# Kernel optimization log

Measured on AMD Instinct MI355X. Metric: run time of the kernel, lower is better.

## Reference

```python
import jax, jax.numpy as jnp
import numpy as np
from jax import lax

S, B, D, H, NQ = 512, 2048, 128, 8, 8  # seq, batch, input_dim, hidden_dim(=n_qubits), n_qubits
EPS = 1e-5


def _qexp(theta):
    """Closed-form PauliZ expectations of the RY-ladder + CNOT-ring circuit.
    <Z_0> = prod_{j=1..n-1} cos(theta_j); <Z_i> = prod_{j=0..i} cos(theta_j) for i>=1.
    theta: [..., NQ] -> [..., NQ]."""
    c = jnp.cos(theta)
    cp = jnp.cumprod(c, axis=-1)                                  # cp[...,i] = prod_{0..i}
    out0 = jnp.prod(c[..., 1:], axis=-1, keepdims=True)           # prod_{1..n-1}
    return jnp.concatenate([out0, cp[..., 1:]], axis=-1)


def _layernorm(x, g, b):
    mu = jnp.mean(x, axis=-1, keepdims=True)
    var = jnp.mean(jnp.square(x - mu), axis=-1, keepdims=True)
    return (x - mu) * lax.rsqrt(var + EPS) * g + b


def setup_inputs() -> dict:
    key = jax.random.key(0)
    ks = jax.random.split(key, 10)
    inputs = jax.random.normal(ks[0], (S, B, D), jnp.float32)
    conv_w = jax.random.normal(ks[1], (H, D, 3), jnp.float32) * (1.0 / np.sqrt(3 * D))
    ln_g = jnp.ones((2 * H,), jnp.float32)
    ln_b = jnp.zeros((2 * H,), jnp.float32)

    def lin(k):
        k1, k2 = jax.random.split(k)
        W = jax.random.normal(k1, (NQ, 2 * H), jnp.float32) * (1.0 / np.sqrt(2 * H))
        b = jax.random.normal(k2, (NQ,), jnp.float32) * 0.05
        return W, b

    Wf, bf = lin(ks[2]); Wi, bi = lin(ks[3]); Wg, bg = lin(ks[4]); Wo, bo = lin(ks[5])
    return dict(inputs=inputs, conv_w=conv_w, ln_g=ln_g, ln_b=ln_b,
                Wf=Wf, bf=bf, Wi=Wi, bi=bi, Wg=Wg, bg=bg, Wo=Wo, bo=bo)


def reference(inputs, conv_w, ln_g, ln_b, Wf, bf, Wi, bi, Wg, bg, Wo, bo):
    # encoder: Conv1d(k=3, pad=1, no bias) over the sequence axis
    x = jnp.transpose(inputs, (1, 2, 0))                           # [B, D, S]
    enc = lax.conv_general_dilated(x, conv_w, window_strides=(1,), padding='SAME',
                                   dimension_numbers=('NCW', 'OIW', 'NCW'))  # [B, H, S]
    enc = jnp.transpose(enc, (2, 0, 1))                            # [S, B, H]

    hx0 = jnp.zeros((B, H), inputs.dtype)
    cx0 = jnp.zeros((B, H), inputs.dtype)

    def step(carry, x_t):
        hx, cx = carry
        comb = _layernorm(jnp.concatenate([x_t, hx], axis=1), ln_g, ln_b)  # [B, 2H]
        f = jax.nn.sigmoid(_qexp(comb @ Wf.T + bf))
        i = jax.nn.sigmoid(_qexp(comb @ Wi.T + bi))
        g = jnp.tanh(_qexp(comb @ Wg.T + bg))
        o = jax.nn.sigmoid(_qexp(comb @ Wo.T + bo))
        # dropout is identity in eval mode
        cx = f * cx + i * g
        hx = o * jnp.tanh(cx)
        return (hx, cx), hx

    (hx, cx), outputs = lax.scan(step, (hx0, cx0), enc)
    return outputs, hx, cx
```

## Files before the change

### kernel.cpp

```cpp
#include <hip/hip_runtime.h>

#define SS 512
#define BB 2048
#define DD 128
#define HH 8

template<int CTRL>
__device__ __forceinline__ float dppf(float old_, float src) {
  return __int_as_float(__builtin_amdgcn_update_dpp(
      __float_as_int(old_), __float_as_int(src), CTRL, 0xF, 0xF, false));
}

__global__ void kw_transpose(const float* __restrict__ w, float* __restrict__ wt) {
  int i = blockIdx.x * blockDim.x + threadIdx.x;
  if (i < 3 * DD * HH) {
    int k = i >> 10;
    int d = (i >> 3) & 127;
    int h = i & 7;
    wt[i] = w[h * (DD * 3) + d * 3 + k];
  }
}

__global__ __launch_bounds__(256) void kconv(const float* __restrict__ x,
                                             const float* __restrict__ wt,
                                             float* __restrict__ enc) {
  const int b = blockIdx.x * 256 + threadIdx.x;
  const int s = blockIdx.y;
  float acc0=0.f,acc1=0.f,acc2=0.f,acc3=0.f,acc4=0.f,acc5=0.f,acc6=0.f,acc7=0.f;

  auto proc = [&](float xe, const float* w8) {
    float4 wa = *(const float4*)(w8);
    float4 wb = *(const float4*)(w8 + 4);
    acc0 = fmaf(xe, wa.x, acc0); acc1 = fmaf(xe, wa.y, acc1);
    acc2 = fmaf(xe, wa.z, acc2); acc3 = fmaf(xe, wa.w, acc3);
    acc4 = fmaf(xe, wb.x, acc4); acc5 = fmaf(xe, wb.y, acc5);
    acc6 = fmaf(xe, wb.z, acc6); acc7 = fmaf(xe, wb.w, acc7);
  };

  #pragma unroll
  for (int k = 0; k < 3; ++k) {
    int sr = s + k - 1;
    if (sr >= 0 && sr < SS) {
      const float* xr = x + ((size_t)sr * BB + b) * DD;
      const float* wk = wt + k * (DD * HH);
      #pragma unroll 4
      for (int d = 0; d < DD; d += 4) {
        float4 xv = *(const float4*)(xr + d);
        const float* wp = wk + d * 8;
        proc(xv.x, wp);
        proc(xv.y, wp + 8);
        proc(xv.z, wp + 16);
        proc(xv.w, wp + 24);
      }
    }
  }
  float4* op = (float4*)(enc + ((size_t)s * BB + b) * HH);
  op[0] = make_float4(acc0, acc1, acc2, acc3);
  op[1] = make_float4(acc4, acc5, acc6, acc7);
}

__global__ __launch_bounds__(64) void krec(
    const float* __restrict__ ln_g, const float* __restrict__ ln_b,
    const float* __restrict__ Wf, const float* __restrict__ bf,
    const float* __restrict__ Wi, const float* __restrict__ bi,
    const float* __restrict__ Wg, const float* __restrict__ bg,
    const float* __restrict__ Wo, const float* __restrict__ bo,
    float* __restrict__ out)
{
  const int tid  = threadIdx.x;
  const int sub  = tid & 31;
  const int gate = sub >> 3;
  const int q    = sub & 7;
  const int b    = blockIdx.x * 2 + (tid >> 5);

  const float* Wm = (gate == 0) ? Wf : (gate == 1) ? Wi : (gate == 2) ? Wg : Wo;
  const float* bm = (gate == 0) ? bf : (gate == 1) ? bi : (gate == 2) ? bg : bo;

  float wraw[16];
  #pragma unroll
  for (int j = 0; j < 16; ++j) wraw[j] = Wm[q * 16 + j];
  float SWp = 0.f, bb = bm[q];
  #pragma unroll
  for (int j = 0; j < 16; ++j) {
    SWp += wraw[j] * ln_g[j];
    bb  = fmaf(ln_b[j], wraw[j], bb);
  }
  float wx[8], wh[8];
  #pragma unroll
  for (int j = 0; j < 8; ++j) wx[j] = wraw[j] * ln_g[j];
  #pragma unroll
  for (int k = 0; k < 8; ++k) { int src = 8 + (q ^ k); wh[k] = wraw[src] * ln_g[src]; }

  const bool  isG  = (gate == 2);
  const float ymul = isG ? 2.f : 1.f;
  const bool  gb0  = (gate & 1) != 0;
  const bool  gb1  = (gate & 2) != 0;

  float h_own = 0.f, c_own = 0.f;
  float r0=0.f,r1=0.f,r2=0.f,r3=0.f,r4=0.f,r5=0.f,r6=0.f,r7=0.f;

  const float4* pl = (const float4*)out + (size_t)b * 2;
  float4 cv0 = pl[0], cv1 = pl[1];
  float* pst = out + (size_t)b * 8 + q;

  for (int s = 0; s < SS; ++s) {
    const float x0=cv0.x, x1=cv0.y, x2=cv0.z, x3=cv0.w;
    const float x4=cv1.x, x5=cv1.y, x6=cv1.z, x7=cv1.w;
    if (s + 1 < SS) {
      pl += BB * 2;
      cv0 = pl[0]; cv1 = pl[1];
    }
    float sv = (((x0+x1)+(x2+x3)) + ((x4+x5)+(x6+x7)))
             + (((r0+r1)+(r2+r3)) + ((r4+r5)+(r6+r7)));
    float qa = fmaf(x0,x0, x1*x1) + fmaf(x2,x2, x3*x3);
    float qb = fmaf(x4,x4, x5*x5) + fmaf(x6,x6, x7*x7);
    float qc = fmaf(r0,r0, r1*r1) + fmaf(r2,r2, r3*r3);
    float qd = fmaf(r4,r4, r5*r5) + fmaf(r6,r6, r7*r7);
    float sq  = (qa + qb) + (qc + qd);
    float mu  = sv * 0.0625f;
    float var = fmaf(-mu, mu, sq * 0.0625f);
    float rinv = __builtin_amdgcn_rsqf(var + 1e-5f);
    float d0 = fmaf(x0,wx[0], x1*wx[1]); d0 = fmaf(x2,wx[2], d0); d0 = fmaf(x3,wx[3], d0);
    float d1 = fmaf(x4,wx[4], x5*wx[5]); d1 = fmaf(x6,wx[6], d1); d1 = fmaf(x7,wx[7], d1);
    float d2 = fmaf(r0,wh[0], r1*wh[1]); d2 = fmaf(r2,wh[2], d2); d2 = fmaf(r3,wh[3], d2);
    float d3 = fmaf(r4,wh[4], r5*wh[5]); d3 = fmaf(r6,wh[6], d3); d3 = fmaf(r7,wh[7], d3);
    float dot = (d0 + d1) + (d2 + d3);
    float theta = fmaf(fmaf(-mu, SWp, dot), rinv, bb);
    float c = __cosf(theta);
    float cp = (q == 0) ? 1.f : c;
    float t;
    t = dppf<0x111>(cp, cp); cp = (q >= 1) ? cp * t : cp;
    t = dppf<0x112>(cp, cp); cp = (q >= 2) ? cp * t : cp;
    t = dppf<0x114>(cp, cp); cp = (q >= 4) ? cp * t : cp;
    float cb  = dppf<0x00>(c, c);
    float cb2 = dppf<0x114>(cb, cb);
    float c0b = (q >= 4) ? cb2 : cb;
    float tot = dppf<0x141>(cp, cp);
    float outq = (q == 0) ? tot : c0b * cp;
    float e  = __expf(-(outq * ymul));
    float sg = __builtin_amdgcn_rcpf(1.f + e);
    float a  = isG ? fmaf(2.f, sg, -1.f) : sg;
    float t1 = dppf<0x128>(a, a);
    float t2 = __shfl_xor(a, 16);
    float t3 = __shfl_xor(t1, 16);
    float v01  = gb0 ? t1 : a;
    float v23  = gb0 ? t3 : t2;
    float v01i = gb0 ? a  : t1;
    float v23i = gb0 ? t2 : t3;
    float fv = gb1 ? v23  : v01;
    float gv = gb1 ? v01  : v23;
    float iv = gb1 ? v23i : v01i;
    float ov = gb1 ? v01i : v23i;
    c_own = fmaf(fv, c_own, iv * gv);
    float e2 = __expf(-2.f * c_own);
    float th = fmaf(2.f, __builtin_amdgcn_rcpf(1.f + e2), -1.f);
    h_own = ov * th;
    if (gate == 0) *pst = h_own;
    pst += BB * HH;
    r0 = h_own;
    r1 = dppf<0xB1>(r0, r0);
    r2 = dppf<0x4E>(r0, r0);
    r3 = dppf<0x4E>(r1, r1);
    float m0 = dppf<0x141>(r0, r0);
    float m1 = dppf<0x141>(r1, r1);
    float m2 = dppf<0x141>(r2, r2);
    float m3 = dppf<0x141>(r3, r3);
    r4 = dppf<0x1B>(m0, m0);
    r5 = dppf<0x1B>(m1, m1);
    r6 = dppf<0x1B>(m2, m2);
    r7 = dppf<0x1B>(m3, m3);
  }
  if (gate == 0) {
    out[(size_t)SS * BB * HH + (size_t)b * HH + q] = h_own;
    out[(size_t)SS * BB * HH + (size_t)BB * HH + (size_t)b * HH + q] = c_own;
  }
}

extern "C" void kernel_launch(void* const* d_in, const int* in_sizes, int n_in,
                              void* d_out, int out_size, void* d_ws, size_t ws_size,
                              hipStream_t stream) {
  const float* x   = (const float*)d_in[0];
  const float* cw  = (const float*)d_in[1];
  const float* lng = (const float*)d_in[2];
  const float* lnb = (const float*)d_in[3];
  const float* Wf_ = (const float*)d_in[4];
  const float* bf_ = (const float*)d_in[5];
  const float* Wi_ = (const float*)d_in[6];
  const float* bi_ = (const float*)d_in[7];
  const float* Wg_ = (const float*)d_in[8];
  const float* bg_ = (const float*)d_in[9];
  const float* Wo_ = (const float*)d_in[10];
  const float* bo_ = (const float*)d_in[11];
  float* out = (float*)d_out;
  float* wt  = (float*)d_ws;

  kw_transpose<<<12, 256, 0, stream>>>(cw, wt);
  kconv<<<dim3(BB / 256, SS), 256, 0, stream>>>(x, wt, out);
  krec<<<BB / 2, 64, 0, stream>>>(lng, lnb, Wf_, bf_, Wi_, bi_, Wg_, bg_, Wo_, bo_, out);
}
```

Measured before the change: 1.115 ms.

## Restructure conv to load each input row once with rolling accumulators and prefetch deeper in recurrence

The conv kernel now tiles 64 sequence rows per block. Each input row is read once and feeds three rolling accumulators for the three kernel taps, instead of being re-read three times. The weight transpose kernel is removed and weights go into LDS. Lanes split D into 4 chunks, with a DPP/swizzle reduction before the store. The recurrence kernel re-maps lanes so the gate exchange uses permlane32 swap instead of a shuffle, prefetches three timesteps ahead, and slightly rebalances the dot-product trees for ILP.

```diff
diff --git a/kernel.cpp b/kernel.cpp
--- a/kernel.cpp
+++ b/kernel.cpp
@@ -4,6 +4,7 @@
 #define BB 2048
 #define DD 128
 #define HH 8
+#define TS 64
 
 template<int CTRL>
 __device__ __forceinline__ float dppf(float old_, float src) {
@@ -11,52 +12,94 @@
       __float_as_int(old_), __float_as_int(src), CTRL, 0xF, 0xF, false));
 }
 
-__global__ void kw_transpose(const float* __restrict__ w, float* __restrict__ wt) {
-  int i = blockIdx.x * blockDim.x + threadIdx.x;
-  if (i < 3 * DD * HH) {
-    int k = i >> 10;
-    int d = (i >> 3) & 127;
-    int h = i & 7;
-    wt[i] = w[h * (DD * 3) + d * 3 + k];
-  }
+__device__ __forceinline__ float xorswap32(float v, bool hi) {
+#if __has_builtin(__builtin_amdgcn_permlane32_swap)
+  auto r = __builtin_amdgcn_permlane32_swap(__float_as_int(v), __float_as_int(v), false, false);
+  struct { int a, b; } s2;
+  __builtin_memcpy(&s2, &r, 8);
+  return __int_as_float(hi ? s2.a : s2.b);
+#else
+  return __shfl_xor(v, 32);
+#endif
 }
 
 __global__ __launch_bounds__(256) void kconv(const float* __restrict__ x,
-                                             const float* __restrict__ wt,
+                                             const float* __restrict__ cw,
                                              float* __restrict__ enc) {
-  const int b = blockIdx.x * 256 + threadIdx.x;
-  const int s = blockIdx.y;
-  float acc0=0.f,acc1=0.f,acc2=0.f,acc3=0.f,acc4=0.f,acc5=0.f,acc6=0.f,acc7=0.f;
-
-  auto proc = [&](float xe, const float* w8) {
-    float4 wa = *(const float4*)(w8);
-    float4 wb = *(const float4*)(w8 + 4);
-    acc0 = fmaf(xe, wa.x, acc0); acc1 = fmaf(xe, wa.y, acc1);
-    acc2 = fmaf(xe, wa.z, acc2); acc3 = fmaf(xe, wa.w, acc3);
-    acc4 = fmaf(xe, wb.x, acc4); acc5 = fmaf(xe, wb.y, acc5);
-    acc6 = fmaf(xe, wb.z, acc6); acc7 = fmaf(xe, wb.w, acc7);
-  };
-
-  #pragma unroll
-  for (int k = 0; k < 3; ++k) {
-    int sr = s + k - 1;
-    if (sr >= 0 && sr < SS) {
-      const float* xr = x + ((size_t)sr * BB + b) * DD;
-      const float* wk = wt + k * (DD * HH);
-      #pragma unroll 4
-      for (int d = 0; d < DD; d += 4) {
-        float4 xv = *(const float4*)(xr + d);
-        const float* wp = wk + d * 8;
-        proc(xv.x, wp);
-        proc(xv.y, wp + 8);
-        proc(xv.z, wp + 16);
-        proc(xv.w, wp + 24);
-      }
+  __shared__ float wl[3][8][132];
+  const int tid = threadIdx.x;
+  for (int i = tid; i < 3 * DD * HH; i += 256) {
+    int h = i / 384;
+    int rem = i - h * 384;
+    int d = rem / 3;
+    int k = rem - d * 3;
+    wl[k][h][d] = cw[i];
+  }
+  __syncthreads();
+
+  const int lane = tid & 63;
+  const int hl   = lane & 31;
+  const int h    = hl & 7;
+  const int dc   = hl >> 3;
+  const int wv   = tid >> 6;
+  const int b    = blockIdx.x * 8 + wv * 2 + (lane >> 5);
+  const int c0   = blockIdx.y * TS;
+  const int dbase = dc * 32;
+
+  auto loadrow = [&](int r, float4 (&xb)[8]) {
+    if (r >= 0 && r < SS) {
+      const float4* p = (const float4*)(x + ((size_t)r * BB + b) * DD + dbase);
+      #pragma unroll
+      for (int j = 0; j < 8; ++j) xb[j] = p[j];
+    } else {
+      #pragma unroll
+      for (int j = 0; j < 8; ++j) xb[j] = make_float4(0.f, 0.f, 0.f, 0.f);
     }
-  }
-  float4* op = (float4*)(enc + ((size_t)s * BB + b) * HH);
-  op[0] = make_float4(acc0, acc1, acc2, acc3);
-  op[1] = make_float4(acc4, acc5, acc6, acc7);
+  };
+
+  auto dorow = [&](const float4 (&xb)[8], float& am, float& a0, float& ap) {
+    #pragma unroll
+    for (int j = 0; j < 8; ++j) {
+      float4 xv = xb[j];
+      float4 w0 = *(const float4*)&wl[0][h][dbase + 4 * j];
+      float4 w1 = *(const float4*)&wl[1][h][dbase + 4 * j];
+      float4 w2 = *(const float4*)&wl[2][h][dbase + 4 * j];
+      ap = fmaf(xv.x, w0.x, ap); a0 = fmaf(xv.x, w1.x, a0); am = fmaf(xv.x, w2.x, am);
+      ap = fmaf(xv.y, w0.y, ap); a0 = fmaf(xv.y, w1.y, a0); am = fmaf(xv.y, w2.y, am);
+      ap = fmaf(xv.z, w0.z, ap); a0 = fmaf(xv.z, w1.z, a0); am = fmaf(xv.z, w2.z, am);
+      ap = fmaf(xv.w, w0.w, ap); a0 = fmaf(xv.w, w1.w, a0); am = fmaf(xv.w, w2.w, am);
+    }
+  };
+
+  auto redstore = [&](float v, int rout) {
+    float v2 = v + dppf<0x128>(v, v);
+    v2 = v2 + __int_as_float(
+        __builtin_amdgcn_ds_swizzle(__float_as_int(v2), 0x401F));
+    if (hl < 8) enc[((size_t)rout * BB + b) * 8 + h] = v2;
+  };
+
+  float am = 0.f, a0 = 0.f, ap = 0.f;
+  float4 xA[8], xB[8];
+  int r = c0 - 1;
+  loadrow(r, xA);
+
+  auto phase = [&](float4 (&xu)[8], float4 (&xl)[8], float& Am, float& A0, float& Ap) {
+    int rn = r + 1;
+    loadrow(rn <= c0 + TS ? rn : -1, xl);
+    dorow(xu, Am, A0, Ap);
+    if (r > c0) redstore(Am, r - 1);
+    Am = 0.f;
+    ++r;
+  };
+
+  for (int it = 0; it < 11; ++it) {
+    phase(xA, xB, am, a0, ap);
+    phase(xB, xA, a0, ap, am);
+    phase(xA, xB, ap, am, a0);
+    phase(xB, xA, am, a0, ap);
+    phase(xA, xB, a0, ap, am);
+    phase(xB, xA, ap, am, a0);
+  }
 }
 
 __global__ __launch_bounds__(64) void krec(
@@ -67,11 +110,13 @@
     const float* __restrict__ Wo, const float* __restrict__ bo,
     float* __restrict__ out)
 {
-  const int tid  = threadIdx.x;
-  const int sub  = tid & 31;
-  const int gate = sub >> 3;
-  const int q    = sub & 7;
-  const int b    = blockIdx.x * 2 + (tid >> 5);
+  const int lane = threadIdx.x;
+  const int q    = lane & 7;
+  const int gb0i = (lane >> 3) & 1;
+  const int gb1i = (lane >> 5) & 1;
+  const int gate = gb1i * 2 + gb0i;
+  const int b    = blockIdx.x * 2 + ((lane >> 4) & 1);
+  const bool gb0 = gb0i != 0, gb1 = gb1i != 0;
 
   const float* Wm = (gate == 0) ? Wf : (gate == 1) ? Wi : (gate == 2) ? Wg : Wo;
   const float* bm = (gate == 0) ? bf : (gate == 1) ? bi : (gate == 2) ? bg : bo;
@@ -93,38 +138,41 @@
 
   const bool  isG  = (gate == 2);
   const float ymul = isG ? 2.f : 1.f;
-  const bool  gb0  = (gate & 1) != 0;
-  const bool  gb1  = (gate & 2) != 0;
 
   float h_own = 0.f, c_own = 0.f;
   float r0=0.f,r1=0.f,r2=0.f,r3=0.f,r4=0.f,r5=0.f,r6=0.f,r7=0.f;
 
-  const float4* pl = (const float4*)out + (size_t)b * 2;
-  float4 cv0 = pl[0], cv1 = pl[1];
+  const float4* pe = (const float4*)out;
+  size_t base = (size_t)b * 2;
+  float4 A0 = pe[base],            A1 = pe[base + 1];
+  float4 B0 = pe[base + BB*2],     B1 = pe[base + BB*2 + 1];
+  float4 C0 = pe[base + BB*4],     C1 = pe[base + BB*4 + 1];
+  size_t nxt = base + BB*6;
   float* pst = out + (size_t)b * 8 + q;
 
-  for (int s = 0; s < SS; ++s) {
-    const float x0=cv0.x, x1=cv0.y, x2=cv0.z, x3=cv0.w;
-    const float x4=cv1.x, x5=cv1.y, x6=cv1.z, x7=cv1.w;
-    if (s + 1 < SS) {
-      pl += BB * 2;
-      cv0 = pl[0]; cv1 = pl[1];
-    }
+  auto step = [&](float4& u0, float4& u1, int s) {
+    const float x0=u0.x, x1=u0.y, x2=u0.z, x3=u0.w;
+    const float x4=u1.x, x5=u1.y, x6=u1.z, x7=u1.w;
+    if (s + 3 < SS) { u0 = pe[nxt]; u1 = pe[nxt + 1]; nxt += BB*2; }
     float sv = (((x0+x1)+(x2+x3)) + ((x4+x5)+(x6+x7)))
              + (((r0+r1)+(r2+r3)) + ((r4+r5)+(r6+r7)));
     float qa = fmaf(x0,x0, x1*x1) + fmaf(x2,x2, x3*x3);
     float qb = fmaf(x4,x4, x5*x5) + fmaf(x6,x6, x7*x7);
-    float qc = fmaf(r0,r0, r1*r1) + fmaf(r2,r2, r3*r3);
-    float qd = fmaf(r4,r4, r5*r5) + fmaf(r6,r6, r7*r7);
+    float qc = fmaf(r1,r1, r0*r0) + fmaf(r3,r3, r2*r2);
+    float qd = fmaf(r5,r5, r4*r4) + fmaf(r7,r7, r6*r6);
     float sq  = (qa + qb) + (qc + qd);
     float mu  = sv * 0.0625f;
     float var = fmaf(-mu, mu, sq * 0.0625f);
     float rinv = __builtin_amdgcn_rsqf(var + 1e-5f);
-    float d0 = fmaf(x0,wx[0], x1*wx[1]); d0 = fmaf(x2,wx[2], d0); d0 = fmaf(x3,wx[3], d0);
-    float d1 = fmaf(x4,wx[4], x5*wx[5]); d1 = fmaf(x6,wx[6], d1); d1 = fmaf(x7,wx[7], d1);
-    float d2 = fmaf(r0,wh[0], r1*wh[1]); d2 = fmaf(r2,wh[2], d2); d2 = fmaf(r3,wh[3], d2);
-    float d3 = fmaf(r4,wh[4], r5*wh[5]); d3 = fmaf(r6,wh[6], d3); d3 = fmaf(r7,wh[7], d3);
-    float dot = (d0 + d1) + (d2 + d3);
+    float d0  = fmaf(x0,wx[0], x1*wx[1]);
+    float d0b = fmaf(x2,wx[2], x3*wx[3]);
+    float d1  = fmaf(x4,wx[4], x5*wx[5]);
+    float d1b = fmaf(x6,wx[6], x7*wx[7]);
+    float d2  = fmaf(r0,wh[0], r1*wh[1]);
+    float d2b = fmaf(r2,wh[2], r3*wh[3]);
+    float d3  = fmaf(r4,wh[4], r5*wh[5]);
+    float d3b = fmaf(r6,wh[6], r7*wh[7]);
+    float dot = ((d0+d0b)+(d1+d1b)) + ((d2+d2b)+(d3+d3b));
     float theta = fmaf(fmaf(-mu, SWp, dot), rinv, bb);
     float c = __cosf(theta);
     float cp = (q == 0) ? 1.f : c;
@@ -141,8 +189,8 @@
     float sg = __builtin_amdgcn_rcpf(1.f + e);
     float a  = isG ? fmaf(2.f, sg, -1.f) : sg;
     float t1 = dppf<0x128>(a, a);
-    float t2 = __shfl_xor(a, 16);
-    float t3 = __shfl_xor(t1, 16);
+    float t2 = xorswap32(a, gb1);
+    float t3 = xorswap32(t1, gb1);
     float v01  = gb0 ? t1 : a;
     float v23  = gb0 ? t3 : t2;
     float v01i = gb0 ? a  : t1;
@@ -169,7 +217,16 @@
     r5 = dppf<0x1B>(m1, m1);
     r6 = dppf<0x1B>(m2, m2);
     r7 = dppf<0x1B>(m3, m3);
-  }
+  };
+
+  for (int s = 0; s < 510; s += 3) {
+    step(A0, A1, s);
+    step(B0, B1, s + 1);
+    step(C0, C1, s + 2);
+  }
+  step(A0, A1, 510);
+  step(B0, B1, 511);
+
   if (gate == 0) {
     out[(size_t)SS * BB * HH + (size_t)b * HH + q] = h_own;
     out[(size_t)SS * BB * HH + (size_t)BB * HH + (size_t)b * HH + q] = c_own;
@@ -192,9 +249,7 @@
   const float* Wo_ = (const float*)d_in[10];
   const float* bo_ = (const float*)d_in[11];
   float* out = (float*)d_out;
-  float* wt  = (float*)d_ws;
-
-  kw_transpose<<<12, 256, 0, stream>>>(cw, wt);
-  kconv<<<dim3(BB / 256, SS), 256, 0, stream>>>(x, wt, out);
+
+  kconv<<<dim3(BB / 8, SS / TS), 256, 0, stream>>>(x, cw, out);
   krec<<<BB / 2, 64, 0, stream>>>(lng, lnb, Wf_, bf_, Wi_, bi_, Wg_, bg_, Wo_, bo_, out);
 }
```

Measured after the change: 1.349 ms. 1.21x slower.
